# Kernel optimization log

Hardware: AMD Instinct MI355X
Metric: run time of the kernel (lower is better)

The kernel has to match this reference:

```python
import jax, jax.numpy as jnp
import numpy as np

B, T, H = 256, 512, 1024


def _xavier(key, shape, gain=1.0):
    fan_in, fan_out = shape[1], shape[0]
    limit = gain * np.sqrt(6.0 / (fan_in + fan_out))
    return jax.random.uniform(key, shape, jnp.float32, -limit, limit)


def setup_inputs() -> dict:
    key = jax.random.key(0)
    ks = jax.random.split(key, 8)
    x = jax.random.normal(ks[0], (B, T, H), jnp.float32)
    ht = jax.random.normal(ks[1], (B, H), jnp.float32)
    # nn.Linear weights are [out, in]; xavier gain 1.0 for Wz/Uz/Wh/Uh, 1.667 for Wr/Ur
    Wz = _xavier(ks[2], (H, H), 1.0)
    Uz = _xavier(ks[3], (H, H), 1.0)
    Wr = _xavier(ks[4], (H, H), 1.667)
    Ur = _xavier(ks[5], (H, H), 1.667)
    Wh = _xavier(ks[6], (H, H), 1.0)
    Uh = _xavier(ks[7], (H, H), 1.0)
    return {"x": x, "ht": ht, "Wz": Wz, "Uz": Uz, "Wr": Wr, "Ur": Ur, "Wh": Wh, "Uh": Uh}


def reference(x, ht, Wz, Uz, Wr, Ur, Wh, Uh):
    # Precompute the input-side projections for all timesteps in two big GEMMs
    # (same math as per-step Wz(x_i)/Wh(x_i), just batched). Note: the original
    # forward computes a reset gate r but never uses it, so it is omitted —
    # identical output.
    xz = jnp.einsum('bti,oi->tbo', x, Wz)  # [T, B, H]
    xh = jnp.einsum('bti,oi->tbo', x, Wh)  # [T, B, H]

    def step(h, xs):
        xz_t, xh_t = xs
        z = jax.nn.sigmoid(xz_t + h @ Uz.T)
        h_ = jnp.tanh(xh_t + h @ Uh.T)
        h = z * h + (1.0 - z) * h_
        return h, None

    h_final, _ = jax.lax.scan(step, ht, (xz, xh))
    return (h_final, h_final)
```

## Files before the change

kernel.cpp:

```cpp
#include <hip/hip_runtime.h>

typedef unsigned short u16;
typedef unsigned int u32;
typedef __bf16 bf16x8 __attribute__((ext_vector_type(8)));
typedef float f32x4 __attribute__((ext_vector_type(4)));
typedef u16 u16x4 __attribute__((ext_vector_type(4)));
typedef u16 u16x8 __attribute__((ext_vector_type(8)));

#define HDIM 1024
#define BATCH 256
#define TSTEPS 512
#define BT (BATCH * TSTEPS)

__device__ __forceinline__ u16 f2bf(float f) {
  union { float f; u32 u; } v; v.f = f;
  u32 r = v.u + 0x7FFFu + ((v.u >> 16) & 1u);
  return (u16)(r >> 16);
}
__device__ __forceinline__ float bf2f(u16 u) {
  union { u32 u; float f; } v; v.u = ((u32)u) << 16;
  return v.f;
}

__device__ __forceinline__ void gload_lds16(const void* g, void* l) {
  __builtin_amdgcn_global_load_lds(
      (const __attribute__((address_space(1))) unsigned int*)g,
      (__attribute__((address_space(3))) unsigned int*)l, 16, 0, 0);
}

__global__ __launch_bounds__(256) void pack_kernel(
    const float* __restrict__ Wz, const float* __restrict__ Uz,
    const float* __restrict__ Wh, const float* __restrict__ Uh,
    const float* __restrict__ ht,
    u16* __restrict__ Wcat, u16* __restrict__ Ucat,
    float* __restrict__ hf0, u16* __restrict__ hb0)
{
  const long M = 1L << 20;
  long e = ((long)blockIdx.x * 256 + threadIdx.x) * 4;
  const float* src;
  u16* dst;
  if (e < M)            { src = Wz + e;        dst = Wcat + e; }
  else if (e < 2 * M)   { src = Wh + (e - M);  dst = Wcat + e; }
  else if (e < 3 * M)   { src = Uz + (e - 2*M); dst = Ucat + (e - 2*M); }
  else if (e < 4 * M)   { src = Uh + (e - 3*M); dst = Ucat + (e - 2*M); }
  else {
    long j = e - 4 * M;
    float4 v = *(const float4*)(ht + j);
    *(float4*)(hf0 + j) = v;
    u16x4 o = { f2bf(v.x), f2bf(v.y), f2bf(v.z), f2bf(v.w) };
    *(u16x4*)(hb0 + j) = o;
    return;
  }
  float4 v = *(const float4*)src;
  u16x4 o = { f2bf(v.x), f2bf(v.y), f2bf(v.z), f2bf(v.w) };
  *(u16x4*)dst = o;
}

__global__ __launch_bounds__(256) void gemm_xw(
    const float* __restrict__ x, const u16* __restrict__ Wcat,
    u16* __restrict__ xzh)
{
  __shared__ u16 As[128 * 64];
  __shared__ u16 Bs[128 * 64];

  const int NWG = (BT / 128) * (2048 / 128);
  int bid = blockIdx.x;
  int swz = (bid & 7) * (NWG / 8) + (bid >> 3);
  int tm = swz >> 4;
  int tn = swz & 15;
  long m0 = (long)tm * 128;
  int n0 = tn * 128;

  int tid = threadIdx.x;
  int w = tid >> 6, l = tid & 63;
  int wr = (w >> 1) * 64;
  int wc = (w & 1) * 64;

  f32x4 acc[4][4] = {};

  const int arow = tid >> 3;
  const int acol = (tid & 7) * 8;
  const int brow = l >> 3;
  const int bcol = (l & 7) * 8;

  for (int kc = 0; kc < 16; ++kc) {
    int k0 = kc * 64;
#pragma unroll
    for (int j = 0; j < 4; ++j) {
      int r = (w * 4 + j) * 8 + brow;
      gload_lds16(Wcat + (((long)(n0 + r)) << 10) + k0 + bcol,
                  &Bs[(w * 4 + j) * 512]);
    }
    float4 av[4][2];
#pragma unroll
    for (int s = 0; s < 4; ++s) {
      const float* src = x + ((m0 + arow + s * 32) << 10) + k0 + acol;
      av[s][0] = *(const float4*)src;
      av[s][1] = *(const float4*)(src + 4);
    }
#pragma unroll
    for (int s = 0; s < 4; ++s) {
      u16x8 o = { f2bf(av[s][0].x), f2bf(av[s][0].y), f2bf(av[s][0].z), f2bf(av[s][0].w),
                  f2bf(av[s][1].x), f2bf(av[s][1].y), f2bf(av[s][1].z), f2bf(av[s][1].w) };
      *(u16x8*)(As + tid * 8 + s * 2048) = o;
    }
    __syncthreads();
#pragma unroll
    for (int kk = 0; kk < 2; ++kk) {
      int kb = kk * 32 + (l >> 4) * 8;
      int rr = l & 15;
      bf16x8 af[4], bfr[4];
#pragma unroll
      for (int i = 0; i < 4; ++i)
        af[i] = *(const bf16x8*)(As + (wr + i * 16 + rr) * 64 + kb);
#pragma unroll
      for (int j = 0; j < 4; ++j)
        bfr[j] = *(const bf16x8*)(Bs + (wc + j * 16 + rr) * 64 + kb);
#pragma unroll
      for (int i = 0; i < 4; ++i)
#pragma unroll
        for (int j = 0; j < 4; ++j)
          acc[i][j] = __builtin_amdgcn_mfma_f32_16x16x32_bf16(af[i], bfr[j], acc[i][j], 0, 0, 0);
    }
    __syncthreads();
  }

  int rq = (l >> 4) * 4;
  int rc = l & 15;
#pragma unroll
  for (int i = 0; i < 4; ++i) {
#pragma unroll
    for (int r = 0; r < 4; ++r) {
      long m = m0 + wr + i * 16 + rq + r;
      int b = (int)(m >> 9);
      int t = (int)(m & 511);
      u16* dst = xzh + (((long)t * 256 + b) << 11);
#pragma unroll
      for (int j = 0; j < 4; ++j)
        dst[n0 + wc + j * 16 + rc] = f2bf(acc[i][j][r]);
    }
  }
}

__global__ __launch_bounds__(256) void gru_step(
    const u16* __restrict__ Ucat, const u16* __restrict__ xzh_t,
    const u16* __restrict__ hbc, const float* __restrict__ hfc,
    u16* __restrict__ hbn, float* __restrict__ hfn)
{
  __shared__ u16 As[2][32 * 64];
  __shared__ u16 Bzs[2][32 * 64];
  __shared__ u16 Bhs[2][32 * 64];

  int bid = blockIdx.x;
  int swz = (bid & 7) * 32 + (bid >> 3);
  int b0 = (swz >> 5) * 32;
  int o0 = (swz & 31) * 32;

  int tid = threadIdx.x;
  int w = tid >> 6, l = tid & 63;
  int wr = (w >> 1) * 16;
  int wc = (w & 1) * 16;

  f32x4 accZ = {0.f, 0.f, 0.f, 0.f};
  f32x4 accH = {0.f, 0.f, 0.f, 0.f};

  const int srow = l >> 3;
  const int scol = (l & 7) * 8;

#define STAGE(kc, buf) do {                                                          \
    int k0_ = (kc) * 64;                                                             \
    gload_lds16(hbc  + (((long)(b0 + w * 8 + srow)) << 10) + k0_ + scol,             \
                &As[buf][w * 512]);                                                  \
    gload_lds16(Ucat + (((long)(o0 + w * 8 + srow)) << 10) + k0_ + scol,             \
                &Bzs[buf][w * 512]);                                                 \
    gload_lds16(Ucat + (((long)(1024 + o0 + w * 8 + srow)) << 10) + k0_ + scol,      \
                &Bhs[buf][w * 512]);                                                 \
  } while (0)

  STAGE(0, 0);
#pragma unroll
  for (int kc = 0; kc < 16; ++kc) {
    int buf = kc & 1;
    if (kc < 15) {
      STAGE(kc + 1, buf ^ 1);
      asm volatile("s_waitcnt vmcnt(3)" ::: "memory");
    } else {
      asm volatile("s_waitcnt vmcnt(0)" ::: "memory");
    }
    asm volatile("s_barrier" ::: "memory");
#pragma unroll
    for (int kk = 0; kk < 2; ++kk) {
      int kb = kk * 32 + (l >> 4) * 8;
      int rr = l & 15;
      bf16x8 a  = *(const bf16x8*)(&As[buf][(wr + rr) * 64 + kb]);
      bf16x8 bz = *(const bf16x8*)(&Bzs[buf][(wc + rr) * 64 + kb]);
      bf16x8 bh = *(const bf16x8*)(&Bhs[buf][(wc + rr) * 64 + kb]);
      accZ = __builtin_amdgcn_mfma_f32_16x16x32_bf16(a, bz, accZ, 0, 0, 0);
      accH = __builtin_amdgcn_mfma_f32_16x16x32_bf16(a, bh, accH, 0, 0, 0);
    }
    asm volatile("s_barrier" ::: "memory");
  }
#undef STAGE

  int rq = (l >> 4) * 4;
  int rc = l & 15;
  int col = o0 + wc + rc;
#pragma unroll
  for (int r = 0; r < 4; ++r) {
    int bq = b0 + wr + rq + r;
    float xz = bf2f(xzh_t[(((long)bq) << 11) + col]);
    float xh = bf2f(xzh_t[(((long)bq) << 11) + 1024 + col]);
    float hold = hfc[(((long)bq) << 10) + col];
    float zp = accZ[r] + xz;
    float hp = accH[r] + xh;
    float z = 1.f / (1.f + __expf(-zp));
    float hh = tanhf(hp);
    float hnew = z * hold + (1.f - z) * hh;
    hfn[(((long)bq) << 10) + col] = hnew;
    hbn[(((long)bq) << 10) + col] = f2bf(hnew);
  }
}

__global__ __launch_bounds__(256) void copy_out(const float* __restrict__ hf,
                                                float* __restrict__ out)
{
  int i = blockIdx.x * 256 + threadIdx.x;
  float4 v = ((const float4*)hf)[i];
  ((float4*)out)[i] = v;
  ((float4*)(out + BATCH * HDIM))[i] = v;
}

extern "C" void kernel_launch(void* const* d_in, const int* in_sizes, int n_in,
                              void* d_out, int out_size, void* d_ws, size_t ws_size,
                              hipStream_t stream)
{
  const float* x  = (const float*)d_in[0];
  const float* ht = (const float*)d_in[1];
  const float* Wz = (const float*)d_in[2];
  const float* Uz = (const float*)d_in[3];
  const float* Wh = (const float*)d_in[6];
  const float* Uh = (const float*)d_in[7];

  char* ws = (char*)d_ws;
  u16*   xzh  = (u16*)ws;
  u16*   Wcat = (u16*)(ws + 536870912L);
  u16*   Ucat = (u16*)(ws + 536870912L + 4194304L);
  float* hf   = (float*)(ws + 536870912L + 8388608L);
  u16*   hb   = (u16*)(ws + 536870912L + 8388608L + 2097152L);

  pack_kernel<<<4352, 256, 0, stream>>>(Wz, Uz, Wh, Uh, ht, Wcat, Ucat, hf, hb);
  gemm_xw<<<16384, 256, 0, stream>>>(x, Wcat, xzh);

  const long HB = (long)BATCH * HDIM;
  for (int t = 0; t < TSTEPS; ++t) {
    int cur = t & 1, nxt = cur ^ 1;
    gru_step<<<256, 256, 0, stream>>>(Ucat, xzh + (long)t * BATCH * 2048,
                                      hb + cur * HB, hf + cur * HB,
                                      hb + nxt * HB, hf + nxt * HB);
  }
  copy_out<<<256, 256, 0, stream>>>(hf, (float*)d_out);
}
```

Measured before the change: 8.104 ms.

## Fuse GRU timestep launches into one persistent kernel with per-group atomic barriers

Replaces the 512 per-timestep gru_step launches and the copy_out kernel with a single persistent kernel. Each workgroup keeps its 32-column slices of Uz and Uh resident in LDS with XOR swizzling, and synchronises with the other workgroups of its batch group through an acquire/release atomic counter instead of kernel boundaries. Each step uses 32x32x16 MFMA split across waves along K, with an LDS reduction, and the final step writes both outputs directly. This removes launch overhead and the per-step reload of the weights, but adds a spin-wait dependency on all 256 workgroups being co-resident and a serial reduction in wave 0.

```diff
diff --git a/kernel.cpp b/kernel.cpp
--- a/kernel.cpp
+++ b/kernel.cpp
@@ -4,6 +4,7 @@
 typedef unsigned int u32;
 typedef __bf16 bf16x8 __attribute__((ext_vector_type(8)));
 typedef float f32x4 __attribute__((ext_vector_type(4)));
+typedef float f32x16 __attribute__((ext_vector_type(16)));
 typedef u16 u16x4 __attribute__((ext_vector_type(4)));
 typedef u16 u16x8 __attribute__((ext_vector_type(8)));
 
@@ -11,6 +12,7 @@
 #define BATCH 256
 #define TSTEPS 512
 #define BT (BATCH * TSTEPS)
+#define HB_ELEMS (BATCH * HDIM)
 
 __device__ __forceinline__ u16 f2bf(float f) {
   union { float f; u32 u; } v; v.f = f;
@@ -33,8 +35,10 @@
     const float* __restrict__ Wh, const float* __restrict__ Uh,
     const float* __restrict__ ht,
     u16* __restrict__ Wcat, u16* __restrict__ Ucat,
-    float* __restrict__ hf0, u16* __restrict__ hb0)
+    float* __restrict__ hf0, u16* __restrict__ hb0,
+    u32* __restrict__ cnt)
 {
+  if (blockIdx.x == 0 && threadIdx.x < 16) cnt[threadIdx.x] = 0;
   const long M = 1L << 20;
   long e = ((long)blockIdx.x * 256 + threadIdx.x) * 4;
   const float* src;
@@ -142,92 +146,145 @@
   }
 }
 
-__global__ __launch_bounds__(256) void gru_step(
-    const u16* __restrict__ Ucat, const u16* __restrict__ xzh_t,
-    const u16* __restrict__ hbc, const float* __restrict__ hfc,
-    u16* __restrict__ hbn, float* __restrict__ hfn)
+__global__ __launch_bounds__(256) void gru_scan(
+    const u16* __restrict__ Ucat, const u16* __restrict__ xzh,
+    u16* __restrict__ hb, float* __restrict__ hf,
+    u32* __restrict__ cnt, float* __restrict__ outp)
 {
-  __shared__ u16 As[2][32 * 64];
-  __shared__ u16 Bzs[2][32 * 64];
-  __shared__ u16 Bhs[2][32 * 64];
+  __shared__ u16 BL[2][32][1024];
+  __shared__ float red[3][2][1024];
 
   int bid = blockIdx.x;
-  int swz = (bid & 7) * 32 + (bid >> 3);
-  int b0 = (swz >> 5) * 32;
-  int o0 = (swz & 31) * 32;
-
+  int g = bid & 7;
+  int j = bid >> 3;
+  int b0 = g * 32;
+  int o0 = j * 32;
   int tid = threadIdx.x;
-  int w = tid >> 6, l = tid & 63;
-  int wr = (w >> 1) * 16;
-  int wc = (w & 1) * 16;
-
-  f32x4 accZ = {0.f, 0.f, 0.f, 0.f};
-  f32x4 accH = {0.f, 0.f, 0.f, 0.f};
-
-  const int srow = l >> 3;
-  const int scol = (l & 7) * 8;
-
-#define STAGE(kc, buf) do {                                                          \
-    int k0_ = (kc) * 64;                                                             \
-    gload_lds16(hbc  + (((long)(b0 + w * 8 + srow)) << 10) + k0_ + scol,             \
-                &As[buf][w * 512]);                                                  \
-    gload_lds16(Ucat + (((long)(o0 + w * 8 + srow)) << 10) + k0_ + scol,             \
-                &Bzs[buf][w * 512]);                                                 \
-    gload_lds16(Ucat + (((long)(1024 + o0 + w * 8 + srow)) << 10) + k0_ + scol,      \
-                &Bhs[buf][w * 512]);                                                 \
-  } while (0)
-
-  STAGE(0, 0);
-#pragma unroll
-  for (int kc = 0; kc < 16; ++kc) {
-    int buf = kc & 1;
-    if (kc < 15) {
-      STAGE(kc + 1, buf ^ 1);
-      asm volatile("s_waitcnt vmcnt(3)" ::: "memory");
-    } else {
-      asm volatile("s_waitcnt vmcnt(0)" ::: "memory");
-    }
-    asm volatile("s_barrier" ::: "memory");
-#pragma unroll
-    for (int kk = 0; kk < 2; ++kk) {
-      int kb = kk * 32 + (l >> 4) * 8;
-      int rr = l & 15;
-      bf16x8 a  = *(const bf16x8*)(&As[buf][(wr + rr) * 64 + kb]);
-      bf16x8 bz = *(const bf16x8*)(&Bzs[buf][(wc + rr) * 64 + kb]);
-      bf16x8 bh = *(const bf16x8*)(&Bhs[buf][(wc + rr) * 64 + kb]);
-      accZ = __builtin_amdgcn_mfma_f32_16x16x32_bf16(a, bz, accZ, 0, 0, 0);
-      accH = __builtin_amdgcn_mfma_f32_16x16x32_bf16(a, bh, accH, 0, 0, 0);
-    }
-    asm volatile("s_barrier" ::: "memory");
-  }
-#undef STAGE
-
-  int rq = (l >> 4) * 4;
-  int rc = l & 15;
-  int col = o0 + wc + rc;
-#pragma unroll
-  for (int r = 0; r < 4; ++r) {
-    int bq = b0 + wr + rq + r;
-    float xz = bf2f(xzh_t[(((long)bq) << 11) + col]);
-    float xh = bf2f(xzh_t[(((long)bq) << 11) + 1024 + col]);
-    float hold = hfc[(((long)bq) << 10) + col];
-    float zp = accZ[r] + xz;
-    float hp = accH[r] + xh;
-    float z = 1.f / (1.f + __expf(-zp));
-    float hh = tanhf(hp);
-    float hnew = z * hold + (1.f - z) * hh;
-    hfn[(((long)bq) << 10) + col] = hnew;
-    hbn[(((long)bq) << 10) + col] = f2bf(hnew);
-  }
-}
-
-__global__ __launch_bounds__(256) void copy_out(const float* __restrict__ hf,
-                                                float* __restrict__ out)
-{
-  int i = blockIdx.x * 256 + threadIdx.x;
-  float4 v = ((const float4*)hf)[i];
-  ((float4*)out)[i] = v;
-  ((float4*)(out + BATCH * HDIM))[i] = v;
+  int w = tid >> 6;
+  int l = tid & 63;
+  int hi = l >> 5;
+  int col = l & 31;
+  const int colx = (l & 7) << 4;
+
+#pragma unroll 1
+  for (int gate = 0; gate < 2; ++gate) {
+    const u16* src = Ucat + (((long)gate << 20) + ((long)o0 << 10));
+    char* dstbase = (char*)&BL[gate][0][0];
+#pragma unroll
+    for (int i = 0; i < 16; ++i) {
+      int c = i * 256 + tid;
+      int row = c >> 7;
+      int inner = (c & 127) << 4;
+      u16x8 v = *(const u16x8*)(src + row * 1024 + (inner >> 1));
+      *(u16x8*)(dstbase + row * 2048 + (inner ^ ((row & 7) << 4))) = v;
+    }
+  }
+  __syncthreads();
+
+  const char* bz_base = (const char*)&BL[0][0][0] + col * 2048;
+  const char* bh_base = (const char*)&BL[1][0][0] + col * 2048;
+  const int kbase = (w << 9) + (hi << 4);
+
+#pragma unroll 1
+  for (int t = 0; t < TSTEPS; ++t) {
+    int cur = t & 1;
+    const u16* hbC = hb + cur * HB_ELEMS;
+    const float* hfC = hf + cur * HB_ELEMS;
+    u16* hbN = hb + (cur ^ 1) * HB_ELEMS;
+    float* hfN = hf + (cur ^ 1) * HB_ELEMS;
+    const u16* xt = xzh + (long)t * (BATCH * 2048);
+
+    if (t > 0) {
+      if (tid == 0) {
+        u32 target = (u32)(32 * t);
+        while (__hip_atomic_load(cnt + g, __ATOMIC_ACQUIRE,
+                                 __HIP_MEMORY_SCOPE_AGENT) < target) {
+          __builtin_amdgcn_s_sleep(1);
+        }
+      }
+      __syncthreads();
+    }
+
+    bf16x8 a[16];
+    const u16* hrow = hbC + ((long)(b0 + col) << 10) + (w << 8) + (hi << 3);
+#pragma unroll
+    for (int ks = 0; ks < 16; ++ks)
+      a[ks] = *(const bf16x8*)(hrow + ks * 16);
+
+    u16 xzv[16], xhv[16];
+    float holdv[16];
+    if (w == 0) {
+#pragma unroll
+      for (int r = 0; r < 16; ++r) {
+        int row = (r & 3) + ((r >> 2) << 3) + (hi << 2);
+        long bq = b0 + row;
+        xzv[r] = xt[(bq << 11) + o0 + col];
+        xhv[r] = xt[(bq << 11) + 1024 + o0 + col];
+        holdv[r] = hfC[(bq << 10) + o0 + col];
+      }
+    }
+
+    f32x16 accZ = {};
+    f32x16 accH = {};
+#pragma unroll
+    for (int ks = 0; ks < 16; ++ks) {
+      int koff = (kbase + ks * 32) ^ colx;
+      bf16x8 bz = *(const bf16x8*)(bz_base + koff);
+      bf16x8 bh = *(const bf16x8*)(bh_base + koff);
+      accZ = __builtin_amdgcn_mfma_f32_32x32x16_bf16(a[ks], bz, accZ, 0, 0, 0);
+      accH = __builtin_amdgcn_mfma_f32_32x32x16_bf16(a[ks], bh, accH, 0, 0, 0);
+    }
+
+    if (w != 0) {
+      float* rb = &red[w - 1][0][0];
+#pragma unroll
+      for (int q = 0; q < 4; ++q) {
+        f32x4 vz = { accZ[q*4+0], accZ[q*4+1], accZ[q*4+2], accZ[q*4+3] };
+        f32x4 vh = { accH[q*4+0], accH[q*4+1], accH[q*4+2], accH[q*4+3] };
+        *(f32x4*)(rb + q * 256 + l * 4) = vz;
+        *(f32x4*)(rb + 1024 + q * 256 + l * 4) = vh;
+      }
+    }
+    __syncthreads();
+
+    if (w == 0) {
+#pragma unroll
+      for (int i = 0; i < 3; ++i) {
+        const float* rb = &red[i][0][0];
+#pragma unroll
+        for (int q = 0; q < 4; ++q) {
+          f32x4 vz = *(const f32x4*)(rb + q * 256 + l * 4);
+          f32x4 vh = *(const f32x4*)(rb + 1024 + q * 256 + l * 4);
+          accZ[q*4+0] += vz[0]; accZ[q*4+1] += vz[1];
+          accZ[q*4+2] += vz[2]; accZ[q*4+3] += vz[3];
+          accH[q*4+0] += vh[0]; accH[q*4+1] += vh[1];
+          accH[q*4+2] += vh[2]; accH[q*4+3] += vh[3];
+        }
+      }
+      bool last = (t == TSTEPS - 1);
+#pragma unroll
+      for (int r = 0; r < 16; ++r) {
+        int row = (r & 3) + ((r >> 2) << 3) + (hi << 2);
+        long bq = b0 + row;
+        float zp = accZ[r] + bf2f(xzv[r]);
+        float hp = accH[r] + bf2f(xhv[r]);
+        float z = 1.f / (1.f + __expf(-zp));
+        float th = tanhf(hp);
+        float hnew = z * holdv[r] + (1.f - z) * th;
+        if (last) {
+          outp[(bq << 10) + o0 + col] = hnew;
+          outp[(long)HB_ELEMS + (bq << 10) + o0 + col] = hnew;
+        } else {
+          hfN[(bq << 10) + o0 + col] = hnew;
+          hbN[(bq << 10) + o0 + col] = f2bf(hnew);
+        }
+      }
+      if (!last && tid == 0) {
+        __hip_atomic_fetch_add(cnt + g, 1u, __ATOMIC_RELEASE,
+                               __HIP_MEMORY_SCOPE_AGENT);
+      }
+    }
+  }
 }
 
 extern "C" void kernel_launch(void* const* d_in, const int* in_sizes, int n_in,
@@ -244,19 +301,12 @@
   char* ws = (char*)d_ws;
   u16*   xzh  = (u16*)ws;
   u16*   Wcat = (u16*)(ws + 536870912L);
-  u16*   Ucat = (u16*)(ws + 536870912L + 4194304L);
-  float* hf   = (float*)(ws + 536870912L + 8388608L);
-  u16*   hb   = (u16*)(ws + 536870912L + 8388608L + 2097152L);
-
-  pack_kernel<<<4352, 256, 0, stream>>>(Wz, Uz, Wh, Uh, ht, Wcat, Ucat, hf, hb);
+  u16*   Ucat = (u16*)(ws + 541065216L);
+  float* hf   = (float*)(ws + 545259520L);
+  u16*   hb   = (u16*)(ws + 547356672L);
+  u32*   cnt  = (u32*)(ws + 548405248L);
+
+  pack_kernel<<<4352, 256, 0, stream>>>(Wz, Uz, Wh, Uh, ht, Wcat, Ucat, hf, hb, cnt);
   gemm_xw<<<16384, 256, 0, stream>>>(x, Wcat, xzh);
-
-  const long HB = (long)BATCH * HDIM;
-  for (int t = 0; t < TSTEPS; ++t) {
-    int cur = t & 1, nxt = cur ^ 1;
-    gru_step<<<256, 256, 0, stream>>>(Ucat, xzh + (long)t * BATCH * 2048,
-                                      hb + cur * HB, hf + cur * HB,
-                                      hb + nxt * HB, hf + nxt * HB);
-  }
-  copy_out<<<256, 256, 0, stream>>>(hf, (float*)d_out);
-}
+  gru_scan<<<256, 256, 0, stream>>>(Ucat, xzh, hb, hf, cnt, (float*)d_out);
+}
```

Result: slower. 8.799 ms (+8.6%).
